# Optimization experiments

Measured on AMD Instinct MI355X. Metric: run time of the kernel, lower is better.

The kernel has to match this reference:

```python
import jax, jax.numpy as jnp
import numpy as np

B, T = 256, 32
AIN, VIN, TIN = 128, 256, 768
H = 256                     # hidden size for all three LSTM subnets
TW0 = 4                     # layer-1 time window
NW = T // TW0               # 8 layer-1 windows == layer-2 time window
R = 16                      # rank
O0, O1 = 128, 64            # inter_node_out_dims
D1 = TW0 * 3 * H + 1        # 3073
D2 = NW * O0 + 1            # 1025
CONST_BIAS = 0.5
POLY_ORDER = 2              # per-layer (same for both layers here)
POLY_NORM = 1


def setup_inputs() -> dict:
    key = jax.random.key(0)
    ks = iter(jax.random.split(key, 32))
    def n(shape, std):
        return jax.random.normal(next(ks), shape, jnp.float32) * std
    def xav(fan_in, fan_out):
        return (2.0 / (fan_in + fan_out)) ** 0.5
    inp = {
        'audio_x': n((B, T, AIN), 1.0),
        'video_x': n((B, T, VIN), 1.0),
        'text_x':  n((B, T, TIN), 1.0),
        # LSTM params (PyTorch layout: W_ih (4H,in), W_hh (4H,H), gate order i,f,g,o)
        'aw_ih': n((4 * H, AIN), xav(AIN, H)), 'aw_hh': n((4 * H, H), xav(H, H)),
        'ab_ih': jnp.zeros((4 * H,), jnp.float32), 'ab_hh': jnp.zeros((4 * H,), jnp.float32),
        'vw_ih': n((4 * H, VIN), xav(VIN, H)), 'vw_hh': n((4 * H, H), xav(H, H)),
        'vb_ih': jnp.zeros((4 * H,), jnp.float32), 'vb_hh': jnp.zeros((4 * H,), jnp.float32),
        'txw_ih': n((4 * H, TIN), xav(TIN, H)), 'txw_hh': n((4 * H, H), xav(H, H)),
        'txb_ih': jnp.zeros((4 * H,), jnp.float32), 'txb_hh': jnp.zeros((4 * H,), jnp.float32),
        # stacked per-window PTP params (one ParameterList entry per window in torch)
        'l1_factor': n((NW, R, D1, O0), xav(D1, O0)),
        'l1_weight': n((NW, R), xav(1, R)),
        'l1_bias': jnp.zeros((NW, O0), jnp.float32),
        'l2_factor': n((1, R, D2, O1), xav(D2, O1)),
        'l2_weight': n((1, R), xav(1, R)),
        'l2_bias': jnp.zeros((1, O1), jnp.float32),
    }
    return inp


def _lstm(x, w_ih, w_hh, b_ih, b_hh):
    """Single-layer batch_first LSTM, zero init state (SubNet in eval: dropout off)."""
    Hh = w_hh.shape[1]
    xp = jnp.einsum('bti,gi->btg', x, w_ih) + b_ih + b_hh          # (B,T,4H)
    def step(carry, xt):
        h, c = carry
        g = xt + h @ w_hh.T
        i, f, gg, o = jnp.split(g, 4, axis=-1)
        i = jax.nn.sigmoid(i); f = jax.nn.sigmoid(f); o = jax.nn.sigmoid(o)
        gg = jnp.tanh(gg)
        c = f * c + i * gg
        h = o * jnp.tanh(c)
        return (h, c), h
    Bb = x.shape[0]
    init = (jnp.zeros((Bb, Hh), x.dtype), jnp.zeros((Bb, Hh), x.dtype))
    _, hs = jax.lax.scan(step, init, xp.transpose(1, 0, 2))         # (T,B,H)
    return hs.transpose(1, 0, 2)


def _ptp(nodes, tw, factor, weight, bias):
    """One ptp_layer with a single modal group; all time windows vectorized.
    nodes: (B,T,F) concat over modalities; factor (nW,R,D,O); weight (nW,R); bias (nW,O).
    """
    Bb, Tt, F = nodes.shape
    nw = Tt // tw
    x = nodes.reshape(Bb, nw, tw * F)
    const = jnp.full((Bb, nw, 1), CONST_BIAS, x.dtype)
    x = jnp.concatenate([const, x], axis=2)                         # (B,nW,D)
    z = jnp.einsum('bnd,nrdo->nbro', x, factor)                     # (nW,B,R,O)
    p = z
    for _ in range(POLY_ORDER):                                     # z^(order+1)
        p = p * z
    for _ in range(POLY_NORM):                                      # sign-sqrt norm
        p = jnp.sign(p) * jnp.sqrt(jnp.abs(p))
    p = p / jnp.linalg.norm(p, axis=-1, keepdims=True)              # euclid_norm
    out = jnp.einsum('nr,nbro->nbo', weight, p) + bias[:, None, :]  # (nW,B,O)
    return out.transpose(1, 0, 2)                                   # (B,nW,O)


def reference(audio_x, video_x, text_x,
              aw_ih, aw_hh, ab_ih, ab_hh,
              vw_ih, vw_hh, vb_ih, vb_hh,
              txw_ih, txw_hh, txb_ih, txb_hh,
              l1_factor, l1_weight, l1_bias,
              l2_factor, l2_weight, l2_bias):
    ah = _lstm(audio_x, aw_ih, aw_hh, ab_ih, ab_hh)
    vh = _lstm(video_x, vw_ih, vw_hh, vb_ih, vb_hh)
    th = _lstm(text_x, txw_ih, txw_hh, txb_ih, txb_hh)
    # modal_win==3: data_dict order is text('0'), audio('1'), video('2');
    # per-window torch.cat along feature dim == concat once over full time axis.
    cat1 = jnp.concatenate([th, ah, vh], axis=2)                    # (B,T,3H)
    f1 = _ptp(cat1, TW0, l1_factor, l1_weight, l1_bias)             # (B,NW,O0)
    f2 = _ptp(f1, NW, l2_factor, l2_weight, l2_bias)                # (B,1,O1)
    return f2.reshape(-1, O1)                                       # (B,O1)
```

## Files before the change

kernel.cpp:

```cpp
#include <hip/hip_runtime.h>
#include <hip/hip_bf16.h>


namespace {
constexpr int kB  = 256;
constexpr int kT  = 32;
constexpr int kH  = 256;
constexpr int k4H = 1024;
constexpr int kNW = 8;
constexpr int kR  = 16;
constexpr int kO0 = 128;
constexpr int kO1 = 64;
constexpr int kD1 = 3073;
constexpr int kD2 = 1025;
}

typedef __attribute__((ext_vector_type(8))) short short8;
typedef __attribute__((ext_vector_type(4))) float f32x4;
typedef __attribute__((ext_vector_type(4))) unsigned int u32x4;

typedef const __attribute__((address_space(1))) unsigned int* gas_u32p;
typedef __attribute__((address_space(3))) unsigned int* las_u32p;

__device__ __forceinline__ unsigned int pack2bf(float a, float b) {
    unsigned int ua = __builtin_bit_cast(unsigned int, a);
    unsigned int ub = __builtin_bit_cast(unsigned int, b);
    return (ua >> 16) | (ub & 0xffff0000u);
}
__device__ __forceinline__ float bflo(unsigned int u) {
    return __builtin_bit_cast(float, u << 16);
}
__device__ __forceinline__ float bfhi(unsigned int u) {
    return __builtin_bit_cast(float, u & 0xffff0000u);
}
__device__ __forceinline__ float sigm(float x) {
    return 1.f / (1.f + __expf(-x));
}
__device__ __forceinline__ float tanh_fast(float x) {
    float a = fabsf(x);
    float t = 1.f - 2.f / (__expf(2.f * a) + 1.f);
    return copysignf(t, x);
}
__device__ __forceinline__ uint2 gload2u(const unsigned short* p) {
    uint2 r;
    asm volatile("global_load_dwordx2 %0, %1, off" : "=v"(r) : "v"(p) : "memory");
    return r;
}

__global__ __launch_bounds__(512)
void k_mm_all(const float* __restrict__ A0, const float* __restrict__ A1,
              const float* __restrict__ A2,
              const float* __restrict__ W0, const float* __restrict__ W1,
              const float* __restrict__ W2,
              const float* __restrict__ bi0, const float* __restrict__ bi1,
              const float* __restrict__ bi2,
              const float* __restrict__ bh0, const float* __restrict__ bh1,
              const float* __restrict__ bh2,
              unsigned short* __restrict__ C0, unsigned short* __restrict__ C1,
              unsigned short* __restrict__ C2,
              const float* __restrict__ wa, const float* __restrict__ wv,
              const float* __restrict__ wtx, unsigned int* __restrict__ wfrag) {
    const int bx  = blockIdx.x;
    const int tid = threadIdx.x;

    if (bx >= 768) {
        int g = (bx - 768) * 512 + tid;
        int l  = g & 63;
        int gt = (g >> 6) & 3;
        int s  = (g >> 8) & 7;
        int w  = (g >> 11) & 15;
        int net = g >> 15;
        const float* W = (net == 0) ? wa : (net == 1) ? wv : wtx;
        const int col = gt * 256 + w * 16 + (l & 15);
        const int k0  = s * 32 + (l >> 4) * 8;
        const float* src = W + (size_t)col * 256 + k0;
        float4 f0 = *(const float4*)src;
        float4 f1 = *(const float4*)(src + 4);
        u32x4 v = { pack2bf(f0.x, f0.y), pack2bf(f0.z, f0.w),
                    pack2bf(f1.x, f1.y), pack2bf(f1.z, f1.w) };
        *(u32x4*)&wfrag[(size_t)g * 4] = v;
        return;
    }

    const int net = bx >> 8;
    const int mt  = (bx & 255) >> 3;
    const int nt  = bx & 7;
    const float* A  = (net == 0) ? A0 : (net == 1) ? A1 : A2;
    const float* W  = (net == 0) ? W0 : (net == 1) ? W1 : W2;
    const float* b1 = (net == 0) ? bi0 : (net == 1) ? bi1 : bi2;
    const float* b2 = (net == 0) ? bh0 : (net == 1) ? bh1 : bh2;
    unsigned short* C = (net == 0) ? C0 : (net == 1) ? C1 : C2;
    const int K = (net == 0) ? 128 : (net == 1) ? 256 : 768;

    __shared__ __align__(16) unsigned int As[256 * 20];
    __shared__ __align__(16) unsigned int Bs[128 * 20];
    const int lane = tid & 63;
    const int wid  = tid >> 6;
    const int wm   = wid >> 1, wn = wid & 1;
    const int m0 = mt * 256, n0 = nt * 128;
    const int nstep = K >> 5;

    const int ar = tid >> 1, akq = (tid & 1) * 16;
    const int br = tid >> 2, bkq = (tid & 3) * 8;
    const float* ap = A + (size_t)(m0 + ar) * K + akq;
    const int nn = n0 + br;
    const int worow = (nn & 3) * 256 + (nn >> 6) * 16 + ((nn >> 2) & 15);
    const float* wp = W + (size_t)worow * K + bkq;

    float4 aR[4], bR[2];
    auto loadA = [&](int s) {
#pragma unroll
        for (int i = 0; i < 4; ++i) aR[i] = *(const float4*)(ap + s * 32 + i * 4);
    };
    auto loadB = [&](int s) {
#pragma unroll
        for (int i = 0; i < 2; ++i) bR[i] = *(const float4*)(wp + s * 32 + i * 4);
    };

    f32x4 acc[4][4];
#pragma unroll
    for (int i = 0; i < 4; ++i)
#pragma unroll
        for (int j = 0; j < 4; ++j) acc[i][j] = (f32x4){0.f, 0.f, 0.f, 0.f};

    loadA(0); loadB(0);
    for (int s = 0; s < nstep; ++s) {
        __syncthreads();
        {
            u32x4 w0 = { pack2bf(aR[0].x, aR[0].y), pack2bf(aR[0].z, aR[0].w),
                         pack2bf(aR[1].x, aR[1].y), pack2bf(aR[1].z, aR[1].w) };
            u32x4 w1 = { pack2bf(aR[2].x, aR[2].y), pack2bf(aR[2].z, aR[2].w),
                         pack2bf(aR[3].x, aR[3].y), pack2bf(aR[3].z, aR[3].w) };
            *(u32x4*)&As[ar * 20 + (akq >> 1)]     = w0;
            *(u32x4*)&As[ar * 20 + (akq >> 1) + 4] = w1;
            u32x4 v0 = { pack2bf(bR[0].x, bR[0].y), pack2bf(bR[0].z, bR[0].w),
                         pack2bf(bR[1].x, bR[1].y), pack2bf(bR[1].z, bR[1].w) };
            *(u32x4*)&Bs[br * 20 + (bkq >> 1)] = v0;
        }
        __syncthreads();
        if (s + 1 < nstep) { loadA(s + 1); loadB(s + 1); }
        short8 af[4], bf[4];
#pragma unroll
        for (int i = 0; i < 4; ++i)
            af[i] = __builtin_bit_cast(short8,
                *(const u32x4*)&As[(wm * 64 + i * 16 + (lane & 15)) * 20 + (lane >> 4) * 4]);
#pragma unroll
        for (int j = 0; j < 4; ++j)
            bf[j] = __builtin_bit_cast(short8,
                *(const u32x4*)&Bs[(wn * 64 + j * 16 + (lane & 15)) * 20 + (lane >> 4) * 4]);
#pragma unroll
        for (int i = 0; i < 4; ++i)
#pragma unroll
            for (int j = 0; j < 4; ++j)
                acc[i][j] = __builtin_amdgcn_mfma_f32_16x16x32_bf16(af[i], bf[j], acc[i][j], 0, 0, 0);
    }
#pragma unroll
    for (int i = 0; i < 4; ++i) {
#pragma unroll
        for (int j = 0; j < 4; ++j) {
            const int col  = n0 + wn * 64 + j * 16 + (lane & 15);
            const int ocol = (col & 3) * 256 + (col >> 6) * 16 + ((col >> 2) & 15);
            const float badd = b1[ocol] + b2[ocol];
#pragma unroll
            for (int e = 0; e < 4; ++e) {
                const int row = m0 + wm * 64 + i * 16 + (lane >> 4) * 4 + e;
                const float v = acc[i][j][e] + badd;
                C[(size_t)row * 1024 + col] =
                    (unsigned short)(__builtin_bit_cast(unsigned int, v) >> 16);
            }
        }
    }
}

__global__ __launch_bounds__(1024, 4)
void k_lstm6(const unsigned short* __restrict__ xp_a, const unsigned short* __restrict__ xp_v,
             const unsigned short* __restrict__ xp_t, const unsigned int* __restrict__ wfrag,
             unsigned short* __restrict__ hp) {
    const int bg  = blockIdx.x;
    const int net = blockIdx.y;
    const int tid = threadIdx.x;
    const int l   = tid & 63;
    const int w   = tid >> 6;
    const unsigned short* xp = (net == 0) ? xp_a : (net == 1) ? xp_v : xp_t;
    const int coloff = (net == 0) ? 256 : (net == 1) ? 512 : 0;

    __shared__ __align__(16) unsigned short hA[8192];
    __shared__ __align__(16) unsigned int Wring[32768];

    for (int i = tid; i < 4096; i += 1024) ((unsigned int*)hA)[i] = 0u;

    const int q  = l & 15;
    const int r0 = (l >> 4) * 4;
    const int d  = w * 16 + q;

    const char* wbase = (const char*)wfrag + (size_t)(net * 16 + w) * 32768 + l * 16;
    unsigned int* wslot = &Wring[w * 2048];

    const unsigned short* xr0 = xp + ((size_t)(bg * 16 + r0) * 32) * 1024 + w * 64 + q * 4;

    const unsigned int rbase = (unsigned int)q * 512;
    const unsigned int rxor  = (unsigned int)(q & 7) << 4;
    const unsigned int kofs  = (unsigned int)(l >> 4) * 16;

    float cc[4] = {0.f, 0.f, 0.f, 0.f};

    auto issue_slab = [&](int slab, int slot) {
#pragma unroll
        for (int g = 0; g < 4; ++g) {
            const void* gp = (const void*)(wbase + slab * 4096 + g * 1024);
            void* lp = (void*)(wslot + slot * 1024 + g * 256);
            __builtin_amdgcn_global_load_lds(
                (gas_u32p)(size_t)gp,
                (las_u32p)(unsigned int)(size_t)lp, 16, 0, 0);
        }
    };

    issue_slab(0, 0);
    issue_slab(1, 1);
    asm volatile("s_waitcnt lgkmcnt(0)" ::: "memory");
    __builtin_amdgcn_s_barrier();

    for (int t = 0; t < kT; ++t) {
        const unsigned short* xr = xr0 + (size_t)t * 1024;
        uint2 xq0 = gload2u(xr);
        uint2 xq1 = gload2u(xr + 32768);
        uint2 xq2 = gload2u(xr + 65536);
        uint2 xq3 = gload2u(xr + 98304);

        const unsigned int rbuf = (unsigned int)(t & 1) * 8192;
        const unsigned int wbuf = 8192u - rbuf;

        f32x4 acc[4];
#pragma unroll
        for (int g = 0; g < 4; ++g) acc[g] = (f32x4){0.f, 0.f, 0.f, 0.f};

#pragma unroll
        for (int s = 0; s < 8; ++s) {
            if (s < 2) asm volatile("s_waitcnt vmcnt(8)" ::: "memory");
            else       asm volatile("s_waitcnt vmcnt(4)" ::: "memory");
            __builtin_amdgcn_sched_barrier(0);
            u32x4 af = *(const u32x4*)((const char*)hA + rbuf + rbase
                                       + (((unsigned)(s * 64) + kofs) ^ rxor));
            const unsigned int* wp = wslot + (s & 1) * 1024;
            u32x4 b0 = *(const u32x4*)(wp + 0 * 256 + l * 4);
            u32x4 b1 = *(const u32x4*)(wp + 1 * 256 + l * 4);
            u32x4 b2 = *(const u32x4*)(wp + 2 * 256 + l * 4);
            u32x4 b3 = *(const u32x4*)(wp + 3 * 256 + l * 4);
            acc[0] = __builtin_amdgcn_mfma_f32_16x16x32_bf16(
                __builtin_bit_cast(short8, af), __builtin_bit_cast(short8, b0), acc[0], 0, 0, 0);
            acc[1] = __builtin_amdgcn_mfma_f32_16x16x32_bf16(
                __builtin_bit_cast(short8, af), __builtin_bit_cast(short8, b1), acc[1], 0, 0, 0);
            acc[2] = __builtin_amdgcn_mfma_f32_16x16x32_bf16(
                __builtin_bit_cast(short8, af), __builtin_bit_cast(short8, b2), acc[2], 0, 0, 0);
            acc[3] = __builtin_amdgcn_mfma_f32_16x16x32_bf16(
                __builtin_bit_cast(short8, af), __builtin_bit_cast(short8, b3), acc[3], 0, 0, 0);
            __builtin_amdgcn_sched_barrier(0);
            issue_slab((s + 2) & 7, s & 1);
        }

        asm volatile("s_waitcnt vmcnt(8)" ::: "memory");
        __builtin_amdgcn_sched_barrier(0);

        float hv[4];
        {
            float gi, gf, gg, go;
            gi = acc[0][0] + bflo(xq0.x); gf = acc[1][0] + bfhi(xq0.x);
            gg = acc[2][0] + bflo(xq0.y); go = acc[3][0] + bfhi(xq0.y);
            cc[0] = sigm(gf) * cc[0] + sigm(gi) * tanh_fast(gg); hv[0] = sigm(go) * tanh_fast(cc[0]);
            gi = acc[0][1] + bflo(xq1.x); gf = acc[1][1] + bfhi(xq1.x);
            gg = acc[2][1] + bflo(xq1.y); go = acc[3][1] + bfhi(xq1.y);
            cc[1] = sigm(gf) * cc[1] + sigm(gi) * tanh_fast(gg); hv[1] = sigm(go) * tanh_fast(cc[1]);
            gi = acc[0][2] + bflo(xq2.x); gf = acc[1][2] + bfhi(xq2.x);
            gg = acc[2][2] + bflo(xq2.y); go = acc[3][2] + bfhi(xq2.y);
            cc[2] = sigm(gf) * cc[2] + sigm(gi) * tanh_fast(gg); hv[2] = sigm(go) * tanh_fast(cc[2]);
            gi = acc[0][3] + bflo(xq3.x); gf = acc[1][3] + bfhi(xq3.x);
            gg = acc[2][3] + bflo(xq3.y); go = acc[3][3] + bfhi(xq3.y);
            cc[3] = sigm(gf) * cc[3] + sigm(gi) * tanh_fast(gg); hv[3] = sigm(go) * tanh_fast(cc[3]);
        }

        const int kk = (t & 3) * 768 + coloff + d;
        const int sp2 = kk >> 5;
        unsigned short* hpb = hp +
            ((((size_t)((t >> 2) * 96 + sp2) * 16 + bg) * 64
              + (unsigned)(r0 | (((kk >> 3) & 3) << 4))) * 8 + (kk & 7));
#pragma unroll
        for (int e = 0; e < 4; ++e) {
            const unsigned short hb =
                (unsigned short)(__builtin_bit_cast(unsigned int, hv[e]) >> 16);
            const int row = r0 + e;
            *(unsigned short*)((char*)hA + wbuf + (unsigned)row * 512
                               + (((unsigned)(2 * d)) ^ (((unsigned)(row & 7)) << 4))) = hb;
            hpb[e * 8] = hb;
        }
        asm volatile("s_waitcnt lgkmcnt(0)" ::: "memory");
        __builtin_amdgcn_s_barrier();
    }
}

__global__ __launch_bounds__(512)
void k_ptp1_mfma(const unsigned int* __restrict__ hp, const float* __restrict__ factor,
                 float* __restrict__ z1) {
    __shared__ __align__(16) unsigned char Bs[64 * 144];
    const int tid  = threadIdx.x;
    const int lane = tid & 63;
    const int wid  = tid >> 6;
    const int r  = blockIdx.x;
    const int n  = blockIdx.y;
    const int bz = blockIdx.z;

    const int bo = tid & 63;
    const int bc = tid >> 6;
    const float* fp = factor + ((size_t)(n * kR + r) * kD1 + 1 + bc * 8) * kO0 + bz * 64 + bo;
    const unsigned int* ha = hp + (size_t)n * 96 * 4096 + lane * 4;

    f32x4 acc[2][4];
#pragma unroll
    for (int i = 0; i < 2; ++i)
#pragma unroll
        for (int j = 0; j < 4; ++j) acc[i][j] = (f32x4){0.f, 0.f, 0.f, 0.f};

    u32x4 pkb[2];
    u32x4 af[2][2][2];
    auto loadB = [&](int s, int qq) {
        float rv[8];
#pragma unroll
        for (int e = 0; e < 8; ++e)
            rv[e] = fp[((size_t)s * 64 + e) * kO0];
        pkb[qq] = (u32x4){ pack2bf(rv[0], rv[1]), pack2bf(rv[2], rv[3]),
                           pack2bf(rv[4], rv[5]), pack2bf(rv[6], rv[7]) };
    };
    auto loadA = [&](int s, int qq) {
#pragma unroll
        for (int ks = 0; ks < 2; ++ks)
#pragma unroll
            for (int i = 0; i < 2; ++i)
                af[qq][ks][i] = *(const u32x4*)(ha
                    + ((size_t)(s * 32 + ks * 16 + wid * 2 + i)) * 256);
    };
    loadB(0, 0); loadA(0, 0);
#pragma unroll 2
    for (int s = 0; s < 48; ++s) {
        const int qq = s & 1;
        __syncthreads();
        *(u32x4*)(Bs + bo * 144 + bc * 16) = pkb[qq];
        __syncthreads();
        if (s + 1 < 48) { loadB(s + 1, qq ^ 1); loadA(s + 1, qq ^ 1); }
        short8 bf[2][4];
#pragma unroll
        for (int ks = 0; ks < 2; ++ks)
#pragma unroll
            for (int j = 0; j < 4; ++j)
                bf[ks][j] = __builtin_bit_cast(short8,
                    *(const u32x4*)(Bs + (j * 16 + (lane & 15)) * 144
                                    + ks * 64 + (lane >> 4) * 16));
#pragma unroll
        for (int ks = 0; ks < 2; ++ks)
#pragma unroll
            for (int i = 0; i < 2; ++i)
#pragma unroll
                for (int j = 0; j < 4; ++j)
                    acc[i][j] = __builtin_amdgcn_mfma_f32_16x16x32_bf16(
                        __builtin_bit_cast(short8, af[qq][ks][i]), bf[ks][j],
                        acc[i][j], 0, 0, 0);
    }
    const size_t zb = (size_t)n * 256;
#pragma unroll
    for (int i = 0; i < 2; ++i) {
#pragma unroll
        for (int j = 0; j < 4; ++j) {
            const int col = bz * 64 + j * 16 + (lane & 15);
#pragma unroll
            for (int e = 0; e < 4; ++e) {
                const int row = (wid * 2 + i) * 16 + (lane >> 4) * 4 + e;
                z1[((zb + row) * kR + r) * kO0 + col] = acc[i][j][e];
            }
        }
    }
}

__global__ __launch_bounds__(64)
void k_ptp1_post(const float* __restrict__ z1, const float* __restrict__ factor,
                 const float* __restrict__ w, const float* __restrict__ bias,
                 float* __restrict__ f1) {
    const int b = blockIdx.x;
    const int n = blockIdx.y;
    const int o = threadIdx.x;
    float sv0[kR], sv1[kR], nrm[kR];
    const size_t zbase = ((size_t)n * kB + b) * kR * kO0;
#pragma unroll
    for (int r = 0; r < kR; ++r) {
        const size_t zo = zbase + r * kO0 + o;
        const size_t fo = (size_t)(n * kR + r) * kD1 * kO0 + o;
        float v0 = z1[zo] + 0.5f * factor[fo];
        float v1 = z1[zo + 64] + 0.5f * factor[fo + 64];
        float a0 = fabsf(v0), a1 = fabsf(v1);
        float s0 = copysignf(a0 * sqrtf(a0), v0);
        float s1 = copysignf(a1 * sqrtf(a1), v1);
        sv0[r] = s0; sv1[r] = s1;
        float t = s0 * s0 + s1 * s1;
#pragma unroll
        for (int off = 1; off < 64; off <<= 1) t += __shfl_xor(t, off, 64);
        nrm[r] = sqrtf(t);
    }
    float out0 = bias[n * kO0 + o];
    float out1 = bias[n * kO0 + o + 64];
#pragma unroll
    for (int r = 0; r < kR; ++r) {
        const float wr = w[n * kR + r];
        out0 += wr * sv0[r] / nrm[r];
        out1 += wr * sv1[r] / nrm[r];
    }
    f1[((size_t)b * kNW + n) * kO0 + o] = out0;
    f1[((size_t)b * kNW + n) * kO0 + o + 64] = out1;
}

__global__ __launch_bounds__(256)
void k_ptp2_gemm(const float* __restrict__ f1flat, const float* __restrict__ factor2,
                 float* __restrict__ z2) {
    const int b0 = blockIdx.x * 32;
    const int r  = blockIdx.y;
    const int tx = threadIdx.x & 63;
    const int ty = threadIdx.x >> 6;
    __shared__ float xs[32][128];
    __shared__ float Fs[128][64];
    float acc[8];
#pragma unroll
    for (int i = 0; i < 8; ++i) acc[i] = 0.f;
    const float* F = factor2 + (size_t)r * kD2 * kO1;

    for (int k0 = 0; k0 < kD2; k0 += 128) {
        const int len = min(128, kD2 - k0);
        {
            const int row = threadIdx.x >> 3;
            const int c0  = (threadIdx.x & 7) * 16;
#pragma unroll
            for (int i = 0; i < 16; ++i) {
                int k = k0 + c0 + i;
                float v = (k == 0) ? 0.5f
                        : (k < kD2 ? f1flat[(size_t)(b0 + row) * 1024 + (k - 1)] : 0.f);
                xs[row][c0 + i] = v;
            }
        }
        {
#pragma unroll
            for (int i = 0; i < 8; ++i) {
                const int u  = threadIdx.x + i * 256;
                const int dd = u >> 4;
                const int oc = (u & 15) * 4;
                float4 v = (k0 + dd < kD2)
                    ? *(const float4*)(F + (size_t)(k0 + dd) * kO1 + oc)
                    : make_float4(0.f, 0.f, 0.f, 0.f);
                *(float4*)&Fs[dd][oc] = v;
            }
        }
        __syncthreads();
        for (int dd = 0; dd < len; ++dd) {
            float wv = Fs[dd][tx];
#pragma unroll
            for (int i = 0; i < 8; ++i) acc[i] = fmaf(xs[ty * 8 + i][dd], wv, acc[i]);
        }
        __syncthreads();
    }
#pragma unroll
    for (int i = 0; i < 8; ++i) {
        const int b = b0 + ty * 8 + i;
        z2[((size_t)b * kR + r) * kO1 + tx] = acc[i];
    }
}

__global__ __launch_bounds__(64)
void k_ptp2_post(const float* __restrict__ z2, const float* __restrict__ w2,
                 const float* __restrict__ b2, float* __restrict__ out) {
    const int b = blockIdx.x;
    const int o = threadIdx.x;
    float sv[kR], nrm[kR];
#pragma unroll
    for (int r = 0; r < kR; ++r) {
        float v = z2[((size_t)b * kR + r) * kO1 + o];
        float a = fabsf(v);
        float s = copysignf(a * sqrtf(a), v);
        sv[r] = s;
        float t = s * s;
#pragma unroll
        for (int off = 1; off < 64; off <<= 1) t += __shfl_xor(t, off, 64);
        nrm[r] = sqrtf(t);
    }
    float acc = b2[o];
#pragma unroll
    for (int r = 0; r < kR; ++r) acc += w2[r] * sv[r] / nrm[r];
    out[(size_t)b * kO1 + o] = acc;
}

extern "C" void kernel_launch(void* const* d_in, const int* in_sizes, int n_in,
                              void* d_out, int out_size, void* d_ws, size_t ws_size,
                              hipStream_t stream) {
    const float* audio_x  = (const float*)d_in[0];
    const float* video_x  = (const float*)d_in[1];
    const float* text_x   = (const float*)d_in[2];
    const float* aw_ih    = (const float*)d_in[3];
    const float* aw_hh    = (const float*)d_in[4];
    const float* ab_ih    = (const float*)d_in[5];
    const float* ab_hh    = (const float*)d_in[6];
    const float* vw_ih    = (const float*)d_in[7];
    const float* vw_hh    = (const float*)d_in[8];
    const float* vb_ih    = (const float*)d_in[9];
    const float* vb_hh    = (const float*)d_in[10];
    const float* txw_ih   = (const float*)d_in[11];
    const float* txw_hh   = (const float*)d_in[12];
    const float* txb_ih   = (const float*)d_in[13];
    const float* txb_hh   = (const float*)d_in[14];
    const float* l1_factor = (const float*)d_in[15];
    const float* l1_weight = (const float*)d_in[16];
    const float* l1_bias   = (const float*)d_in[17];
    const float* l2_factor = (const float*)d_in[18];
    const float* l2_weight = (const float*)d_in[19];
    const float* l2_bias   = (const float*)d_in[20];

    float* ws = (float*)d_ws;
    unsigned short* xp_a = (unsigned short*)ws;
    unsigned short* xp_v = (unsigned short*)(ws + 4194304);
    unsigned short* xp_t = (unsigned short*)(ws + 8388608);
    unsigned short* hp   = (unsigned short*)(ws + 12582912);
    unsigned int* wfrag  = (unsigned int*)(ws + 15728640);
    float* z1 = ws;
    float* f1 = ws + 8388608;
    float* z2 = ws + 8388608 + 262144;

    k_mm_all<<<960, 512, 0, stream>>>(audio_x, video_x, text_x,
                                      aw_ih, vw_ih, txw_ih,
                                      ab_ih, vb_ih, txb_ih,
                                      ab_hh, vb_hh, txb_hh,
                                      xp_a, xp_v, xp_t,
                                      aw_hh, vw_hh, txw_hh, wfrag);

    k_lstm6<<<dim3(16, 3), 1024, 0, stream>>>(xp_a, xp_v, xp_t, wfrag, hp);

    k_ptp1_mfma<<<dim3(16, 8, 2), 512, 0, stream>>>((const unsigned int*)hp, l1_factor, z1);
    k_ptp1_post<<<dim3(256, 8), 64, 0, stream>>>(z1, l1_factor, l1_weight, l1_bias, f1);

    k_ptp2_gemm<<<dim3(8, 16), 256, 0, stream>>>(f1, l2_factor, z2);
    k_ptp2_post<<<256, 64, 0, stream>>>(z2, l2_weight, l2_bias, (float*)d_out);
}
```

Before: 419.1 us.

## Fuse LSTM recurrence with layer-1 PTP GEMM using per-window completion flags

Merges the LSTM kernel and the layer-1 PTP MFMA GEMM into one launch. 48 blocks run the recurrence and bump a per-window atomic flag after every fourth timestep. The other 208 blocks spin on those flags and compute that window's GEMM tiles while later timesteps are still running. This hides the PTP1 GEMM behind the serial LSTM and removes one launch. It relies on all LSTM blocks being co-resident with the spinning blocks, moves z1 to a new workspace offset, and the flags are reset by the first kernel.

```diff
diff --git a/kernel.cpp b/kernel.cpp
--- a/kernel.cpp
+++ b/kernel.cpp
@@ -59,11 +59,13 @@
               unsigned short* __restrict__ C0, unsigned short* __restrict__ C1,
               unsigned short* __restrict__ C2,
               const float* __restrict__ wa, const float* __restrict__ wv,
-              const float* __restrict__ wtx, unsigned int* __restrict__ wfrag) {
+              const float* __restrict__ wtx, unsigned int* __restrict__ wfrag,
+              unsigned int* __restrict__ flags) {
     const int bx  = blockIdx.x;
     const int tid = threadIdx.x;
 
     if (bx >= 768) {
+        if (bx == 768 && tid < 8) flags[tid] = 0u;
         int g = (bx - 768) * 512 + tid;
         int l  = g & 63;
         int gt = (g >> 6) & 3;
@@ -173,19 +175,116 @@
 }
 
 __global__ __launch_bounds__(1024, 4)
-void k_lstm6(const unsigned short* __restrict__ xp_a, const unsigned short* __restrict__ xp_v,
-             const unsigned short* __restrict__ xp_t, const unsigned int* __restrict__ wfrag,
-             unsigned short* __restrict__ hp) {
-    const int bg  = blockIdx.x;
-    const int net = blockIdx.y;
+void k_lstm_ptp1(const unsigned short* __restrict__ xp_a, const unsigned short* __restrict__ xp_v,
+                 const unsigned short* __restrict__ xp_t, const unsigned int* __restrict__ wfrag,
+                 unsigned short* __restrict__ hp, const float* __restrict__ factor,
+                 float* __restrict__ z1, unsigned int* __restrict__ flags) {
+    __shared__ __align__(16) unsigned short hA[8192];
+    __shared__ __align__(16) unsigned int Wring[32768];
+
+    const int bx  = blockIdx.x;
     const int tid = threadIdx.x;
+
+    if (bx >= 48) {
+        if (tid >= 512) return;
+        unsigned char* Bs = (unsigned char*)hA;
+        const int lane = tid & 63;
+        const int wid  = tid >> 6;
+        const int bo = tid & 63;
+        const int bc = tid >> 6;
+
+        for (int ti = bx - 48; ti < 256; ti += 208) {
+            const int n  = ti >> 5;
+            const int r  = (ti >> 1) & 15;
+            const int bz = ti & 1;
+
+            if (tid == 0) {
+                while (__hip_atomic_load(&flags[n], __ATOMIC_ACQUIRE,
+                                         __HIP_MEMORY_SCOPE_AGENT) < 48u)
+                    __builtin_amdgcn_s_sleep(32);
+            }
+            __syncthreads();
+            __builtin_amdgcn_fence(__ATOMIC_ACQUIRE, "agent");
+
+            const float* fp = factor
+                + ((size_t)(n * kR + r) * kD1 + 1 + bc * 8) * kO0 + bz * 64 + bo;
+            const unsigned int* ha = (const unsigned int*)hp
+                + (size_t)n * 96 * 4096 + lane * 4;
+
+            f32x4 acc[2][4];
+#pragma unroll
+            for (int i = 0; i < 2; ++i)
+#pragma unroll
+                for (int j = 0; j < 4; ++j) acc[i][j] = (f32x4){0.f, 0.f, 0.f, 0.f};
+
+            u32x4 pkb[2];
+            u32x4 af[2][2][2];
+            auto loadB = [&](int s, int qq) {
+                float rv[8];
+#pragma unroll
+                for (int e = 0; e < 8; ++e)
+                    rv[e] = fp[((size_t)s * 64 + e) * kO0];
+                pkb[qq] = (u32x4){ pack2bf(rv[0], rv[1]), pack2bf(rv[2], rv[3]),
+                                   pack2bf(rv[4], rv[5]), pack2bf(rv[6], rv[7]) };
+            };
+            auto loadA = [&](int s, int qq) {
+#pragma unroll
+                for (int ks = 0; ks < 2; ++ks)
+#pragma unroll
+                    for (int i = 0; i < 2; ++i)
+                        af[qq][ks][i] = *(const u32x4*)(ha
+                            + ((size_t)(s * 32 + ks * 16 + wid * 2 + i)) * 256);
+            };
+            loadB(0, 0); loadA(0, 0);
+#pragma unroll 2
+            for (int s = 0; s < 48; ++s) {
+                const int qq = s & 1;
+                __syncthreads();
+                *(u32x4*)(Bs + bo * 144 + bc * 16) = pkb[qq];
+                __syncthreads();
+                if (s + 1 < 48) { loadB(s + 1, qq ^ 1); loadA(s + 1, qq ^ 1); }
+                short8 bf[2][4];
+#pragma unroll
+                for (int ks = 0; ks < 2; ++ks)
+#pragma unroll
+                    for (int j = 0; j < 4; ++j)
+                        bf[ks][j] = __builtin_bit_cast(short8,
+                            *(const u32x4*)(Bs + (j * 16 + (lane & 15)) * 144
+                                            + ks * 64 + (lane >> 4) * 16));
+#pragma unroll
+                for (int ks = 0; ks < 2; ++ks)
+#pragma unroll
+                    for (int i = 0; i < 2; ++i)
+#pragma unroll
+                        for (int j = 0; j < 4; ++j)
+                            acc[i][j] = __builtin_amdgcn_mfma_f32_16x16x32_bf16(
+                                __builtin_bit_cast(short8, af[qq][ks][i]), bf[ks][j],
+                                acc[i][j], 0, 0, 0);
+            }
+            const size_t zb = (size_t)n * 256;
+#pragma unroll
+            for (int i = 0; i < 2; ++i) {
+#pragma unroll
+                for (int j = 0; j < 4; ++j) {
+                    const int col = bz * 64 + j * 16 + (lane & 15);
+#pragma unroll
+                    for (int e = 0; e < 4; ++e) {
+                        const int row = (wid * 2 + i) * 16 + (lane >> 4) * 4 + e;
+                        z1[((zb + row) * kR + r) * kO0 + col] = acc[i][j][e];
+                    }
+                }
+            }
+            __syncthreads();
+        }
+        return;
+    }
+
+    const int bg  = bx & 15;
+    const int net = bx >> 4;
     const int l   = tid & 63;
     const int w   = tid >> 6;
     const unsigned short* xp = (net == 0) ? xp_a : (net == 1) ? xp_v : xp_t;
     const int coloff = (net == 0) ? 256 : (net == 1) ? 512 : 0;
-
-    __shared__ __align__(16) unsigned short hA[8192];
-    __shared__ __align__(16) unsigned int Wring[32768];
 
     for (int i = tid; i < 4096; i += 1024) ((unsigned int*)hA)[i] = 0u;
 
@@ -292,89 +391,14 @@
                                + (((unsigned)(2 * d)) ^ (((unsigned)(row & 7)) << 4))) = hb;
             hpb[e * 8] = hb;
         }
+
+        if ((t & 3) == 3)
+            __builtin_amdgcn_fence(__ATOMIC_RELEASE, "agent");
         asm volatile("s_waitcnt lgkmcnt(0)" ::: "memory");
         __builtin_amdgcn_s_barrier();
-    }
-}
-
-__global__ __launch_bounds__(512)
-void k_ptp1_mfma(const unsigned int* __restrict__ hp, const float* __restrict__ factor,
-                 float* __restrict__ z1) {
-    __shared__ __align__(16) unsigned char Bs[64 * 144];
-    const int tid  = threadIdx.x;
-    const int lane = tid & 63;
-    const int wid  = tid >> 6;
-    const int r  = blockIdx.x;
-    const int n  = blockIdx.y;
-    const int bz = blockIdx.z;
-
-    const int bo = tid & 63;
-    const int bc = tid >> 6;
-    const float* fp = factor + ((size_t)(n * kR + r) * kD1 + 1 + bc * 8) * kO0 + bz * 64 + bo;
-    const unsigned int* ha = hp + (size_t)n * 96 * 4096 + lane * 4;
-
-    f32x4 acc[2][4];
-#pragma unroll
-    for (int i = 0; i < 2; ++i)
-#pragma unroll
-        for (int j = 0; j < 4; ++j) acc[i][j] = (f32x4){0.f, 0.f, 0.f, 0.f};
-
-    u32x4 pkb[2];
-    u32x4 af[2][2][2];
-    auto loadB = [&](int s, int qq) {
-        float rv[8];
-#pragma unroll
-        for (int e = 0; e < 8; ++e)
-            rv[e] = fp[((size_t)s * 64 + e) * kO0];
-        pkb[qq] = (u32x4){ pack2bf(rv[0], rv[1]), pack2bf(rv[2], rv[3]),
-                           pack2bf(rv[4], rv[5]), pack2bf(rv[6], rv[7]) };
-    };
-    auto loadA = [&](int s, int qq) {
-#pragma unroll
-        for (int ks = 0; ks < 2; ++ks)
-#pragma unroll
-            for (int i = 0; i < 2; ++i)
-                af[qq][ks][i] = *(const u32x4*)(ha
-                    + ((size_t)(s * 32 + ks * 16 + wid * 2 + i)) * 256);
-    };
-    loadB(0, 0); loadA(0, 0);
-#pragma unroll 2
-    for (int s = 0; s < 48; ++s) {
-        const int qq = s & 1;
-        __syncthreads();
-        *(u32x4*)(Bs + bo * 144 + bc * 16) = pkb[qq];
-        __syncthreads();
-        if (s + 1 < 48) { loadB(s + 1, qq ^ 1); loadA(s + 1, qq ^ 1); }
-        short8 bf[2][4];
-#pragma unroll
-        for (int ks = 0; ks < 2; ++ks)
-#pragma unroll
-            for (int j = 0; j < 4; ++j)
-                bf[ks][j] = __builtin_bit_cast(short8,
-                    *(const u32x4*)(Bs + (j * 16 + (lane & 15)) * 144
-                                    + ks * 64 + (lane >> 4) * 16));
-#pragma unroll
-        for (int ks = 0; ks < 2; ++ks)
-#pragma unroll
-            for (int i = 0; i < 2; ++i)
-#pragma unroll
-                for (int j = 0; j < 4; ++j)
-                    acc[i][j] = __builtin_amdgcn_mfma_f32_16x16x32_bf16(
-                        __builtin_bit_cast(short8, af[qq][ks][i]), bf[ks][j],
-                        acc[i][j], 0, 0, 0);
-    }
-    const size_t zb = (size_t)n * 256;
-#pragma unroll
-    for (int i = 0; i < 2; ++i) {
-#pragma unroll
-        for (int j = 0; j < 4; ++j) {
-            const int col = bz * 64 + j * 16 + (lane & 15);
-#pragma unroll
-            for (int e = 0; e < 4; ++e) {
-                const int row = (wid * 2 + i) * 16 + (lane >> 4) * 4 + e;
-                z1[((zb + row) * kR + r) * kO0 + col] = acc[i][j][e];
-            }
-        }
+        if ((t & 3) == 3 && tid == 0)
+            __hip_atomic_fetch_add(&flags[t >> 2], 1u, __ATOMIC_RELEASE,
+                                   __HIP_MEMORY_SCOPE_AGENT);
     }
 }
 
@@ -522,7 +546,8 @@
     unsigned short* xp_t = (unsigned short*)(ws + 8388608);
     unsigned short* hp   = (unsigned short*)(ws + 12582912);
     unsigned int* wfrag  = (unsigned int*)(ws + 15728640);
-    float* z1 = ws;
+    unsigned int* flags  = (unsigned int*)(ws + 16121856);
+    float* z1 = ws + 16121872;
     float* f1 = ws + 8388608;
     float* z2 = ws + 8388608 + 262144;
 
@@ -531,11 +556,11 @@
                                       ab_ih, vb_ih, txb_ih,
                                       ab_hh, vb_hh, txb_hh,
                                       xp_a, xp_v, xp_t,
-                                      aw_hh, vw_hh, txw_hh, wfrag);
-
-    k_lstm6<<<dim3(16, 3), 1024, 0, stream>>>(xp_a, xp_v, xp_t, wfrag, hp);
-
-    k_ptp1_mfma<<<dim3(16, 8, 2), 512, 0, stream>>>((const unsigned int*)hp, l1_factor, z1);
+                                      aw_hh, vw_hh, txw_hh, wfrag, flags);
+
+    k_lstm_ptp1<<<256, 1024, 0, stream>>>(xp_a, xp_v, xp_t, wfrag, hp,
+                                          l1_factor, z1, flags);
+
     k_ptp1_post<<<dim3(256, 8), 64, 0, stream>>>(z1, l1_factor, l1_weight, l1_bias, f1);
 
     k_ptp2_gemm<<<dim3(8, 16), 256, 0, stream>>>(f1, l2_factor, z2);
```

New measurement: 1.166 ms. 178% more time.
